# Performance work log

Measured on AMD Instinct MI355X. Metric: run time of the kernel, lower is better.

## Reference

```python
import jax, jax.numpy as jnp
import numpy as np
from jax import lax


def _mdlstm_dir(x, Wx, Wh, Wv, b):
    # x: [H, W, B, Cin]; one diagonal-causal 2D-LSTM scan (top-left origin).
    H, W, B, Cin = x.shape
    C = Wh.shape[0]
    xa = jnp.einsum('hwbi,ic->hwbc', x, Wx) + b  # [H,W,B,5C] precomputed input gates

    def col_step(carry, inp):
        h_l, c_l = carry                    # left neighbor [B,C]
        xa_ij, h_u, c_u = inp               # input preact, up neighbor
        a = xa_ij + h_l @ Wh + h_u @ Wv     # [B,5C]
        i, f1, f2, o, g = jnp.split(a, 5, axis=-1)
        c = jax.nn.sigmoid(i) * jnp.tanh(g) + jax.nn.sigmoid(f1) * c_l + jax.nn.sigmoid(f2) * c_u
        h = jax.nn.sigmoid(o) * jnp.tanh(c)
        return (h, c), (h, c)

    z = jnp.zeros((B, C), x.dtype)
    zrow = jnp.zeros((W, B, C), x.dtype)

    def row_step(carry, xa_row):
        h_up, c_up = carry                  # [W,B,C]
        _, (hs, cs) = lax.scan(col_step, (z, z), (xa_row, h_up, c_up))
        return (hs, cs), hs

    _, hh = lax.scan(row_step, (zrow, zrow), xa)  # [H,W,B,C]
    return hh


def _mdlstm4(x, Wx, Wh, Wv, b):
    # x: [B,Cin,H,W] -> per-direction outputs [4,H,W,B,C] (directions: TL, TR, BL, BR origins)
    xt = jnp.transpose(x, (2, 3, 0, 1))  # [H,W,B,Cin]
    x4 = jnp.stack([xt, xt[:, ::-1], xt[::-1], xt[::-1, ::-1]])
    o = jax.vmap(_mdlstm_dir)(x4, Wx, Wh, Wv, b)  # [4,H,W,B,C]
    return jnp.stack([o[0], o[1][:, ::-1], o[2][::-1], o[3][::-1, ::-1]])


def _block(x, Wx, Wh, Wv, b, cw, cb):
    h4 = _mdlstm4(x, Wx, Wh, Wv, b)            # [4,H,W,B,C]
    h = jnp.transpose(h4.sum(0), (2, 3, 0, 1))  # sum directions -> [B,C,H,W]
    y = lax.conv_general_dilated(h, cw, window_strides=(2, 2), padding='VALID',
                                 dimension_numbers=('NCHW', 'OIHW', 'NCHW'))
    return jnp.tanh(y + cb[None, :, None, None])


def _forward(x, p0_Wx, p0_Wh, p0_Wv, p0_b, c0_w, c0_b,
             p1_Wx, p1_Wh, p1_Wv, p1_b, c1_w, c1_b,
             p2_Wx, p2_Wh, p2_Wv, p2_b, dW, db):
    x = _block(x, p0_Wx, p0_Wh, p0_Wv, p0_b, c0_w, c0_b)  # [B,6,31,126]
    x = _block(x, p1_Wx, p1_Wh, p1_Wv, p1_b, c1_w, c1_b)  # [B,20,14,61]
    h4 = _mdlstm4(x, p2_Wx, p2_Wh, p2_Wv, p2_b)           # [4,H,W,B,50]
    # per-direction Linear(50->100) then sum over the 4 directions
    out = jnp.einsum('dhwbc,dcn->bhwn', h4, dW) + db.sum(0)
    return out  # [B,14,61,100]


def setup_inputs() -> dict:
    key = jax.random.key(0)
    ks = jax.random.split(key, 20)
    rn = lambda k, s, sc=0.1: jax.random.normal(k, s, jnp.float32) * sc
    return {
        'x': jax.random.normal(ks[0], (16, 1, 64, 256), jnp.float32),
        'p0_Wx': rn(ks[1], (4, 1, 10)), 'p0_Wh': rn(ks[2], (4, 2, 10)),
        'p0_Wv': rn(ks[3], (4, 2, 10)), 'p0_b': rn(ks[4], (4, 10)),
        'c0_w': rn(ks[5], (6, 2, 2, 4)), 'c0_b': rn(ks[6], (6,)),
        'p1_Wx': rn(ks[7], (4, 6, 50)), 'p1_Wh': rn(ks[8], (4, 10, 50)),
        'p1_Wv': rn(ks[9], (4, 10, 50)), 'p1_b': rn(ks[10], (4, 50)),
        'c1_w': rn(ks[11], (20, 10, 2, 4)), 'c1_b': rn(ks[12], (20,)),
        'p2_Wx': rn(ks[13], (4, 20, 250)), 'p2_Wh': rn(ks[14], (4, 50, 250)),
        'p2_Wv': rn(ks[15], (4, 50, 250)), 'p2_b': rn(ks[16], (4, 250)),
        'dW': rn(ks[17], (4, 50, 100)), 'db': rn(ks[18], (4, 100)),
    }


def reference(x, p0_Wx, p0_Wh, p0_Wv, p0_b, c0_w, c0_b,
              p1_Wx, p1_Wh, p1_Wv, p1_b, c1_w, c1_b,
              p2_Wx, p2_Wh, p2_Wv, p2_b, dW, db):
    return _forward(x, p0_Wx, p0_Wh, p0_Wv, p0_b, c0_w, c0_b,
                    p1_Wx, p1_Wh, p1_Wv, p1_b, c1_w, c1_b,
                    p2_Wx, p2_Wh, p2_Wv, p2_b, dW, db)
```

## Files before the change

### kernel.cpp

```cpp
#include <hip/hip_runtime.h>

typedef unsigned short ushort_t;
typedef __attribute__((ext_vector_type(8))) short short8;
typedef __attribute__((ext_vector_type(4))) float float4_t;
typedef __attribute__((ext_vector_type(2))) float v2f;

__device__ __forceinline__ float frcp(float x) { return __builtin_amdgcn_rcpf(x); }
__device__ __forceinline__ float fsig(float x) { return frcp(1.f + __expf(-x)); }
__device__ __forceinline__ float ftanh(float x) { return 1.f - 2.f * frcp(1.f + __expf(2.f * x)); }
__device__ __forceinline__ float sig_e2(float a) { return frcp(1.f + __builtin_amdgcn_exp2f(a)); }
__device__ __forceinline__ float th_e2(float a) { return 1.f - 2.f * frcp(1.f + __builtin_amdgcn_exp2f(a)); }

__device__ __forceinline__ ushort_t f2bf(float f) {
    union { float f; unsigned u; } v; v.f = f;
    unsigned u = v.u;
    unsigned r = (u + 0x7fffu + ((u >> 16) & 1u)) >> 16;
    return (ushort_t)r;
}
__device__ __forceinline__ float bf2f(ushort_t s) {
    union { unsigned u; float f; } v; v.u = ((unsigned)s) << 16;
    return v.f;
}
__device__ __forceinline__ float dpp_shr1(float x) {
    int i = __builtin_bit_cast(int, x);
    int r = __builtin_amdgcn_update_dpp(0, i, 0x138 , 0xf, 0xf, true);
    return __builtin_bit_cast(float, r);
}

__device__ __forceinline__ void barrier_lds() {
    asm volatile("s_waitcnt lgkmcnt(0)" ::: "memory");
    __builtin_amdgcn_s_barrier();
    asm volatile("" ::: "memory");
}

__global__ __launch_bounds__(128) void k_mdlstm0(
    const float* __restrict__ x, const float* __restrict__ Wx,
    const float* __restrict__ Wh, const float* __restrict__ Wv,
    const float* __restrict__ bias, float* __restrict__ h0)
{
    const int dir = blockIdx.x >> 4, b = blockIdx.x & 15;
    const int tid = threadIdx.x;
    const int u = tid >> 6;
    const int lane = tid & 63;
    const bool fH = dir >= 2, fW = (dir & 1) != 0;
    const int ri = fH ? 63 - lane : lane;
    const float L2E = 1.44269504088896340736f;

    __shared__ float Xs[64 * 256];
    __shared__ float hbuf[2][2][64];
    {
        const float* xg = x + b * 64 * 256;
        for (int i4 = tid; i4 < 4096; i4 += 128) {
            int row = i4 >> 6, c4 = (i4 & 63) << 2;
            float4 v = *(const float4*)(xg + (row << 8) + c4);
            *(float4*)&Xs[(row << 8) + c4] = v;
        }
        for (int i = tid; i < 256; i += 128) ((float*)hbuf)[i] = 0.f;
    }
    __syncthreads();

    float wx[5], bs[5], whS[5], whO[5], wvS[5], wvO[5];
#pragma unroll
    for (int g = 0; g < 5; g++) {
        float sc = (g == 4) ? 2.f * L2E : -L2E;
        int n = g * 2 + u;
        wx[g]  = Wx[dir * 10 + n] * sc;
        bs[g]  = bias[dir * 10 + n] * sc;
        whS[g] = Wh[(dir * 2 + u) * 10 + n] * sc;
        whO[g] = Wh[(dir * 2 + (1 - u)) * 10 + n] * sc;
        wvS[g] = Wv[(dir * 2 + u) * 10 + n] * sc;
        wvO[g] = Wv[(dir * 2 + (1 - u)) * 10 + n] * sc;
    }

    float* orow = h0 + (((dir * 16 + b) * 64 + ri) * 256) * 2 + u;
    float hr = 0.f, cr = 0.f;

    auto ld = [&](int d) -> float {
        int j = d - lane; j = j < 0 ? 0 : (j > 255 ? 255 : j);
        int cj = fW ? 255 - j : j;
        return Xs[(ri << 8) + cj];
    };
    float xp0 = ld(0), xp1 = ld(1);

    int p = 0;
    for (int d = 0; d < 319; d++) {
        float xv = xp0;
        xp0 = xp1;
        xp1 = ld(d + 2);

        float ho  = hbuf[p][1 - u][lane];
        float hus = dpp_shr1(hr);
        float cu  = dpp_shr1(cr);
        float huo = dpp_shr1(ho);

        int j = d - lane;
        if (j >= 0 && j < 256) {
            float a[5];
#pragma unroll
            for (int g = 0; g < 5; g++) {
                float t = fmaf(xv, wx[g], bs[g]);
                t = fmaf(hr,  whS[g], t);
                t = fmaf(ho,  whO[g], t);
                t = fmaf(hus, wvS[g], t);
                t = fmaf(huo, wvO[g], t);
                a[g] = t;
            }
            float si  = sig_e2(a[0]);
            float sf1 = sig_e2(a[1]);
            float sf2 = sig_e2(a[2]);
            float so  = sig_e2(a[3]);
            float tg  = th_e2(a[4]);
            float cn = si * tg + sf1 * cr + sf2 * cu;
            float tc = th_e2(cn * (2.f * L2E));
            hr = so * tc;
            cr = cn;
            int cj = fW ? 255 - j : j;
            orow[cj * 2] = hr;
        } else {
            hr = 0.f;
            cr = 0.f;
        }
        hbuf[1 - p][u][lane] = hr;
        barrier_lds();
        p ^= 1;
    }
}

__global__ __launch_bounds__(128) void k_conv0(
    const float* __restrict__ h0, const float* __restrict__ cw,
    const float* __restrict__ cb, float* __restrict__ x1)
{
    int blk = blockIdx.x;
    int oh = blk / 127, ow = blk % 127;
    int t = threadIdx.x;
    if (t >= 96) return;
    int b = t / 6, co = t % 6;
    float w[2][2][4];
#pragma unroll
    for (int ci = 0; ci < 2; ci++)
#pragma unroll
        for (int kh = 0; kh < 2; kh++)
#pragma unroll
            for (int kw = 0; kw < 4; kw++)
                w[ci][kh][kw] = cw[((co * 2 + ci) * 2 + kh) * 4 + kw];
    float acc = cb[co];
    for (int dirb = 0; dirb < 4; dirb++) {
#pragma unroll
        for (int kh = 0; kh < 2; kh++) {
#pragma unroll
            for (int kw = 0; kw < 4; kw++) {
                const float* ptr = h0 + ((((dirb * 16 + b) * 64) + (2 * oh + kh)) * 256 + (2 * ow + kw)) * 2;
                float2 hv = *(const float2*)ptr;
                acc = fmaf(hv.x, w[0][kh][kw], acc);
                acc = fmaf(hv.y, w[1][kh][kw], acc);
            }
        }
    }
    x1[((oh * 127 + ow) * 16 + b) * 6 + co] = ftanh(acc);
}

__global__ __launch_bounds__(768, 1) void k_mdlstm1(
    const float* __restrict__ x1, const float* __restrict__ Wx,
    const float* __restrict__ Wh, const float* __restrict__ Wv,
    const float* __restrict__ bias, float* __restrict__ h1)
{
    const int dir = blockIdx.x >> 4, b = blockIdx.x & 15;
    const bool fH = dir >= 2, fW = (dir & 1) != 0;
    const int tid = threadIdx.x;
    const int wave = tid >> 6, lane = tid & 63;

    __shared__ float Xs1[32 * 127 * 6];
    __shared__ __align__(16) ushort_t Ah[2][32][40];
    __shared__ __align__(16) ushort_t Al[2][32][40];
    __shared__ float P[32][68];
    __shared__ float cbuf[2][33][12];

    for (int i = tid; i < 2 * 32 * 40; i += 768) { ((ushort_t*)Ah)[i] = 0; ((ushort_t*)Al)[i] = 0; }
    for (int i = tid; i < 2 * 33 * 12; i += 768) ((float*)cbuf)[i] = 0.f;
    for (int i = tid; i < 32 * 127 * 6; i += 768)
        Xs1[i] = x1[(i / 6) * 96 + b * 6 + (i % 6)];
    __syncthreads();
    if (tid < 6) {
        int rr = fH ? 31 : 0, cc = fW ? 126 : 0;
        float xv = Xs1[(rr * 127 + cc) * 6 + tid];
        ushort_t xh = f2bf(xv);
        Ah[0][0][20 + tid] = xh;
        Al[0][0][20 + tid] = f2bf(xv - bf2f(xh));
    }

    const int mt = wave & 1, nt = wave >> 1;
    short8 bh = {0,0,0,0,0,0,0,0}, bl = {0,0,0,0,0,0,0,0};
    if (wave < 8) {
        int n = nt * 16 + (lane & 15);
#pragma unroll
        for (int jj = 0; jj < 8; jj++) {
            int k = (lane >> 4) * 8 + jj;
            float v = 0.f;
            if (n < 50) {
                if (k < 10)      v = Wh[(dir * 10 + k) * 50 + n];
                else if (k < 20) v = Wv[(dir * 10 + (k - 10)) * 50 + n];
                else if (k < 26) v = Wx[(dir * 6 + (k - 20)) * 50 + n];
            }
            ushort_t hi = f2bf(v);
            bh[jj] = (short)hi;
            bl[jj] = (short)f2bf(v - bf2f(hi));
        }
    }

    const int cell = tid / 10, u = tid % 10;
    float br[5];
#pragma unroll
    for (int g = 0; g < 5; g++) br[g] = (tid < 320) ? bias[dir * 50 + g * 10 + u] : 0.f;
    const int ri = fH ? 31 - cell : cell;
    float creg = 0.f;
    __syncthreads();

    int p = 0;
    for (int d = 0; d < 158; d++) {
        if (wave < 8) {
            const int arow = mt * 16 + (lane & 15);
            const int koff = (lane >> 4) * 8;
            short8 ah = *(const short8*)&Ah[p][arow][koff];
            short8 al = *(const short8*)&Al[p][arow][koff];
            float4_t acc = {0.f, 0.f, 0.f, 0.f};
            acc = __builtin_amdgcn_mfma_f32_16x16x32_bf16(ah, bh, acc, 0, 0, 0);
            acc = __builtin_amdgcn_mfma_f32_16x16x32_bf16(al, bh, acc, 0, 0, 0);
            acc = __builtin_amdgcn_mfma_f32_16x16x32_bf16(ah, bl, acc, 0, 0, 0);
            int col = nt * 16 + (lane & 15);
            int r0 = (lane >> 4) * 4;
#pragma unroll
            for (int r = 0; r < 4; r++) P[mt * 16 + r0 + r][col] = acc[r];
        } else if (tid >= 512 && tid < 704) {
            int s = tid - 512, xc = s / 6, ci = s % 6;
            int jn = d + 1 - xc;
            if (jn >= 0 && jn < 127) {
                int rr = fH ? 31 - xc : xc, cc = fW ? 126 - jn : jn;
                float xv = Xs1[(rr * 127 + cc) * 6 + ci];
                ushort_t xh = f2bf(xv);
                Ah[1 - p][xc][20 + ci] = xh;
                Al[1 - p][xc][20 + ci] = f2bf(xv - bf2f(xh));
            }
        }
        barrier_lds();

        if (tid < 320) {
            int j = d - cell;
            if (j >= 0 && j < 127) {
                float ai  = P[cell][u]      + br[0];
                float af1 = P[cell][10 + u] + br[1];
                float af2 = P[cell][20 + u] + br[2];
                float ao  = P[cell][30 + u] + br[3];
                float ag  = P[cell][40 + u] + br[4];
                float cu = cbuf[p][cell][u];
                float cn = fsig(ai) * ftanh(ag) + fsig(af1) * creg + fsig(af2) * cu;
                float hn = fsig(ao) * ftanh(cn);
                creg = cn;
                cbuf[1 - p][cell + 1][u] = cn;
                ushort_t hh = f2bf(hn);
                float hhf = bf2f(hh);
                ushort_t hlo = f2bf(hn - hhf);
                Ah[1 - p][cell][u] = hh;
                Al[1 - p][cell][u] = hlo;
                if (cell < 31) { Ah[1 - p][cell + 1][10 + u] = hh; Al[1 - p][cell + 1][10 + u] = hlo; }
                int cj = fW ? 126 - j : j;
                h1[(((dir * 16 + b) * 32 + ri) * 127 + cj) * 10 + u] = hn;
            }
        }
        barrier_lds();
        p ^= 1;
    }
}

__global__ __launch_bounds__(320, 1) void k_conv1(
    const float* __restrict__ h1, const float* __restrict__ cw,
    const float* __restrict__ cb, float* __restrict__ x2)
{
    int blk = blockIdx.x;
    int oh = blk / 62, ow = blk % 62;
    int t = threadIdx.x;
    int b = t / 20, co = t % 20;
    float w[10][2][4];
#pragma unroll
    for (int ci = 0; ci < 10; ci++)
#pragma unroll
        for (int kh = 0; kh < 2; kh++)
#pragma unroll
            for (int kw = 0; kw < 4; kw++)
                w[ci][kh][kw] = cw[((co * 10 + ci) * 2 + kh) * 4 + kw];
    float acc = cb[co];
    for (int dirb = 0; dirb < 4; dirb++) {
#pragma unroll
        for (int kh = 0; kh < 2; kh++) {
#pragma unroll
            for (int kw = 0; kw < 4; kw++) {
                const float* ptr = h1 + ((((dirb * 16 + b) * 32) + (2 * oh + kh)) * 127 + (2 * ow + kw)) * 10;
#pragma unroll
                for (int ci = 0; ci < 10; ci++)
                    acc = fmaf(ptr[ci], w[ci][kh][kw], acc);
            }
        }
    }
    x2[((oh * 62 + ow) * 16 + b) * 20 + co] = ftanh(acc);
}

__global__ __launch_bounds__(256) void k_prepB2(
    const float* __restrict__ Wh, const float* __restrict__ Wv,
    const float* __restrict__ Wx, ushort_t* __restrict__ Bh,
    ushort_t* __restrict__ Bl)
{
    int idx = blockIdx.x * 256 + threadIdx.x;
    if (idx >= 131072) return;
    int dir = idx >> 15; int k = (idx >> 8) & 127; int n = idx & 255;
    float v = 0.f;
    if (n < 250) {
        if (k < 50)       v = Wh[(dir * 50 + k) * 250 + n];
        else if (k < 100) v = Wv[(dir * 50 + (k - 50)) * 250 + n];
        else if (k < 120) v = Wx[(dir * 20 + (k - 100)) * 250 + n];
    }
    ushort_t hi = f2bf(v);
    Bh[idx] = hi;
    Bl[idx] = f2bf(v - bf2f(hi));
}

__global__ __launch_bounds__(512, 1) void k_mdlstm2(
    const float* __restrict__ x2, const ushort_t* __restrict__ BmH,
    const ushort_t* __restrict__ BmL,
    const float* __restrict__ bias, float* __restrict__ h2)
{
    const int dir = blockIdx.x >> 4, b = blockIdx.x & 15;
    const bool fH = dir >= 2, fW = (dir & 1) != 0;
    const int tid = threadIdx.x;
    const int wave = tid >> 6, lane = tid & 63;

    __shared__ float Xs2[16 * 62 * 20];
    __shared__ __align__(16) ushort_t Ah[2][16][136];
    __shared__ __align__(16) ushort_t Al[2][16][136];
    __shared__ float P[16][260];
    __shared__ float cbuf[2][16][52];

    for (int i = tid; i < 2 * 16 * 136; i += 512) { ((ushort_t*)Ah)[i] = 0; ((ushort_t*)Al)[i] = 0; }
    for (int i = tid; i < 16 * 62 * 20; i += 512)
        Xs2[i] = x2[(i / 20) * 320 + b * 20 + (i % 20)];
    __syncthreads();
    if (tid < 20) {
        int ci = tid;
        int rr = fH ? 15 : 0, cc = fW ? 61 : 0;
        float xv = Xs2[(rr * 62 + cc) * 20 + ci];
        ushort_t xh = f2bf(xv);
        Ah[0][0][100 + ci] = xh;
        Al[0][0][100 + ci] = f2bf(xv - bf2f(xh));
    }

    short8 bfragH[4][4], bfragL[4][4];
    if (wave < 4) {
#pragma unroll
        for (int j = 0; j < 4; j++) {
            const int n = wave * 64 + j * 16 + (lane & 15);
#pragma unroll
            for (int q = 0; q < 4; q++) {
#pragma unroll
                for (int jj = 0; jj < 8; jj++) {
                    int k = q * 32 + (lane >> 4) * 8 + jj;
                    bfragH[j][q][jj] = (short)BmH[(dir * 128 + k) * 256 + n];
                    bfragL[j][q][jj] = (short)BmL[(dir * 128 + k) * 256 + n];
                }
            }
        }
    }

    const int cell0 = tid / 50, u0 = tid % 50;
    const int cell1 = (512 + tid) / 50, u1 = (512 + tid) % 50;
    float bA0 = bias[dir * 250 + u0];
    float bA1 = bias[dir * 250 + 50 + u0];
    float bA2 = bias[dir * 250 + 100 + u0];
    float bA3 = bias[dir * 250 + 150 + u0];
    float bA4 = bias[dir * 250 + 200 + u0];
    float bB0 = 0, bB1 = 0, bB2 = 0, bB3 = 0, bB4 = 0;
    if (tid < 288) {
        bB0 = bias[dir * 250 + u1];
        bB1 = bias[dir * 250 + 50 + u1];
        bB2 = bias[dir * 250 + 100 + u1];
        bB3 = bias[dir * 250 + 150 + u1];
        bB4 = bias[dir * 250 + 200 + u1];
    }
    const int rrc0 = fH ? 15 - cell0 : cell0;
    const int rrc1 = fH ? 15 - cell1 : cell1;
    float creg0 = 0.f, creg1 = 0.f;
    __syncthreads();

    int p = 0;
    for (int d = 0; d < 77; d++) {
        if (wave < 4) {
            const int arow = lane & 15;
            const int koff = (lane >> 4) * 8;
            short8 ah[4], al[4];
#pragma unroll
            for (int q = 0; q < 4; q++) {
                ah[q] = *(const short8*)&Ah[p][arow][q * 32 + koff];
                al[q] = *(const short8*)&Al[p][arow][q * 32 + koff];
            }
            float4_t acc[4];
#pragma unroll
            for (int j = 0; j < 4; j++) acc[j] = (float4_t){0.f, 0.f, 0.f, 0.f};
#pragma unroll
            for (int q = 0; q < 4; q++)
#pragma unroll
                for (int j = 0; j < 4; j++)
                    acc[j] = __builtin_amdgcn_mfma_f32_16x16x32_bf16(ah[q], bfragH[j][q], acc[j], 0, 0, 0);
#pragma unroll
            for (int q = 0; q < 4; q++)
#pragma unroll
                for (int j = 0; j < 4; j++)
                    acc[j] = __builtin_amdgcn_mfma_f32_16x16x32_bf16(al[q], bfragH[j][q], acc[j], 0, 0, 0);
#pragma unroll
            for (int q = 0; q < 4; q++)
#pragma unroll
                for (int j = 0; j < 4; j++)
                    acc[j] = __builtin_amdgcn_mfma_f32_16x16x32_bf16(ah[q], bfragL[j][q], acc[j], 0, 0, 0);
            const int r0 = (lane >> 4) * 4;
#pragma unroll
            for (int j = 0; j < 4; j++) {
                int col = wave * 64 + j * 16 + (lane & 15);
#pragma unroll
                for (int r = 0; r < 4; r++) P[r0 + r][col] = acc[j][r];
            }
        } else {
            int s = tid - 256;
#pragma unroll
            for (int it = 0; it < 2; it++) {
                int item = s + it * 256;
                if (item < 320) {
                    int xc = item / 20, ci = item % 20;
                    int jn = d + 1 - xc;
                    if (jn >= 0 && jn < 62) {
                        int rr = fH ? 15 - xc : xc, cc = fW ? 61 - jn : jn;
                        float xv = Xs2[(rr * 62 + cc) * 20 + ci];
                        ushort_t xh = f2bf(xv);
                        Ah[1 - p][xc][100 + ci] = xh;
                        Al[1 - p][xc][100 + ci] = f2bf(xv - bf2f(xh));
                    }
                }
            }
        }
        barrier_lds();

        auto gate = [&](int j, int cell, int u, int rrc,
                        float g0, float g1, float g2, float g3, float g4,
                        float& creg) {
            float ai  = P[cell][u] + g0;
            float af1 = P[cell][50 + u] + g1;
            float af2 = P[cell][100 + u] + g2;
            float ao  = P[cell][150 + u] + g3;
            float ag  = P[cell][200 + u] + g4;
            float cu = (cell == 0) ? 0.f : cbuf[p][cell - 1][u];
            float cn = fsig(ai) * ftanh(ag) + fsig(af1) * creg + fsig(af2) * cu;
            float hn = fsig(ao) * ftanh(cn);
            creg = cn;
            cbuf[1 - p][cell][u] = cn;
            ushort_t hh = f2bf(hn);
            float hhf = bf2f(hh);
            ushort_t hlo = f2bf(hn - hhf);
            Ah[1 - p][cell][u] = hh;
            Al[1 - p][cell][u] = hlo;
            if (cell < 15) { Ah[1 - p][cell + 1][50 + u] = hh; Al[1 - p][cell + 1][50 + u] = hlo; }
            int cc = fW ? 61 - j : j;
            h2[(((dir * 16 + b) * 16 + rrc) * 62 + cc) * 50 + u] = hn;
        };
        {
            int j0 = d - cell0;
            if (j0 >= 0 && j0 < 62)
                gate(j0, cell0, u0, rrc0, bA0, bA1, bA2, bA3, bA4, creg0);
            if (tid < 288) {
                int j1 = d - cell1;
                if (j1 >= 0 && j1 < 62)
                    gate(j1, cell1, u1, rrc1, bB0, bB1, bB2, bB3, bB4, creg1);
            }
        }
        barrier_lds();
        p ^= 1;
    }
}

__global__ __launch_bounds__(256) void k_final(
    const float* __restrict__ h2, const float* __restrict__ dW,
    const float* __restrict__ db, float* __restrict__ out)
{
    int blk = blockIdx.x;
    int r = blk / 62, c = blk % 62;
    int t = threadIdx.x;
    __shared__ float hb[3200];
    for (int i = t; i < 3200; i += 256) {
        int dirb = i / 800, rem = i % 800, b = rem / 50, u = rem % 50;
        hb[i] = h2[(((dirb * 16 + b) * 16 + r) * 62 + c) * 50 + u];
    }
    __syncthreads();
    for (int o = t; o < 1600; o += 256) {
        int b = o / 100, n = o % 100;
        float acc = db[n] + db[100 + n] + db[200 + n] + db[300 + n];
#pragma unroll
        for (int dirb = 0; dirb < 4; dirb++) {
            const float* hp = hb + (dirb * 16 + b) * 50;
            const float* wp = dW + dirb * 5000 + n;
#pragma unroll 10
            for (int cc2 = 0; cc2 < 50; cc2++)
                acc = fmaf(hp[cc2], wp[cc2 * 100], acc);
        }
        out[((b * 16 + r) * 62 + c) * 100 + n] = acc;
    }
}

extern "C" void kernel_launch(void* const* d_in, const int* in_sizes, int n_in,
                              void* d_out, int out_size, void* d_ws, size_t ws_size,
                              hipStream_t stream)
{
    const float* x     = (const float*)d_in[0];
    const float* p0_Wx = (const float*)d_in[1];
    const float* p0_Wh = (const float*)d_in[2];
    const float* p0_Wv = (const float*)d_in[3];
    const float* p0_b  = (const float*)d_in[4];
    const float* c0_w  = (const float*)d_in[5];
    const float* c0_b  = (const float*)d_in[6];
    const float* p1_Wx = (const float*)d_in[7];
    const float* p1_Wh = (const float*)d_in[8];
    const float* p1_Wv = (const float*)d_in[9];
    const float* p1_b  = (const float*)d_in[10];
    const float* c1_w  = (const float*)d_in[11];
    const float* c1_b  = (const float*)d_in[12];
    const float* p2_Wx = (const float*)d_in[13];
    const float* p2_Wh = (const float*)d_in[14];
    const float* p2_Wv = (const float*)d_in[15];
    const float* p2_b  = (const float*)d_in[16];
    const float* dW    = (const float*)d_in[17];
    const float* db    = (const float*)d_in[18];
    float* out = (float*)d_out;
    float* ws  = (float*)d_ws;

    float* h0 = ws;
    float* x1 = h0 + 2097152;
    float* h1 = x1 + 390144;
    float* x2 = h1 + 2600960;
    float* h2 = x2 + 317440;
    ushort_t* BmH = (ushort_t*)(h2 + 3174400);
    ushort_t* BmL = BmH + 131072;

    k_prepB2<<<512, 256, 0, stream>>>(p2_Wh, p2_Wv, p2_Wx, BmH, BmL);
    k_mdlstm0<<<64, 128, 0, stream>>>(x, p0_Wx, p0_Wh, p0_Wv, p0_b, h0);
    k_conv0<<<32 * 127, 128, 0, stream>>>(h0, c0_w, c0_b, x1);
    k_mdlstm1<<<64, 768, 0, stream>>>(x1, p1_Wx, p1_Wh, p1_Wv, p1_b, h1);
    k_conv1<<<16 * 62, 320, 0, stream>>>(h1, c1_w, c1_b, x2);
    k_mdlstm2<<<64, 512, 0, stream>>>(x2, BmH, BmL, p2_b, h2);
    k_final<<<16 * 62, 256, 0, stream>>>(h2, dW, db, out);
}
```

Baseline: 478.2 us.

## Stage conv inputs in LDS per row/batch and widen mdlstm2 to one gate per thread

Both conv kernels now give each block one output row for one batch. The block stages the needed input rows from all four directions, plus the weights, into shared memory, so the strided global reads are no longer repeated per output pixel. k_mdlstm2 grows from 512 to 832 threads so each of the 800 gate cells has its own thread instead of some threads handling two. The x-staging work is also spread over 320 threads with one item each. The wider block adds register pressure and lengthens barrier waits in the serial diagonal loop. The conv kernels launch far fewer blocks, which reduces parallelism.

```diff
diff --git a/kernel.cpp b/kernel.cpp
--- a/kernel.cpp
+++ b/kernel.cpp
@@ -126,37 +126,43 @@
     }
 }
 
-__global__ __launch_bounds__(128) void k_conv0(
+__global__ __launch_bounds__(256) void k_conv0(
     const float* __restrict__ h0, const float* __restrict__ cw,
     const float* __restrict__ cb, float* __restrict__ x1)
 {
-    int blk = blockIdx.x;
-    int oh = blk / 127, ow = blk % 127;
-    int t = threadIdx.x;
-    if (t >= 96) return;
-    int b = t / 6, co = t % 6;
-    float w[2][2][4];
-#pragma unroll
-    for (int ci = 0; ci < 2; ci++)
-#pragma unroll
-        for (int kh = 0; kh < 2; kh++)
-#pragma unroll
-            for (int kw = 0; kw < 4; kw++)
-                w[ci][kh][kw] = cw[((co * 2 + ci) * 2 + kh) * 4 + kw];
-    float acc = cb[co];
-    for (int dirb = 0; dirb < 4; dirb++) {
-#pragma unroll
-        for (int kh = 0; kh < 2; kh++) {
-#pragma unroll
-            for (int kw = 0; kw < 4; kw++) {
-                const float* ptr = h0 + ((((dirb * 16 + b) * 64) + (2 * oh + kh)) * 256 + (2 * ow + kw)) * 2;
-                float2 hv = *(const float2*)ptr;
-                acc = fmaf(hv.x, w[0][kh][kw], acc);
-                acc = fmaf(hv.y, w[1][kh][kw], acc);
-            }
-        }
-    }
-    x1[((oh * 127 + ow) * 16 + b) * 6 + co] = ftanh(acc);
+    const int oh = blockIdx.x >> 4, b = blockIdx.x & 15;
+    const int tid = threadIdx.x;
+
+    __shared__ float hs[8][512];
+    __shared__ float cws[192];
+
+    for (int i4 = tid; i4 < 1024; i4 += 256) {
+        int dk = i4 >> 7;
+        int c4 = (i4 & 127) << 2;
+        const float* src = h0 + (((dk >> 1) * 16 + b) * 64 + (2 * oh + (dk & 1))) * 512 + c4;
+        *(float4*)&hs[dk][c4] = *(const float4*)src;
+    }
+    if (tid < 192) cws[tid] = cw[tid];
+    __syncthreads();
+
+    for (int o = tid; o < 762; o += 256) {
+        int ow = o / 6, co = o % 6;
+        float acc = cb[co];
+#pragma unroll
+        for (int dirb = 0; dirb < 4; dirb++) {
+#pragma unroll
+            for (int kh = 0; kh < 2; kh++) {
+                const float* hp = &hs[dirb * 2 + kh][0];
+#pragma unroll
+                for (int kw = 0; kw < 4; kw++) {
+                    float2 hv = *(const float2*)&hp[(2 * ow + kw) * 2];
+                    acc = fmaf(hv.x, cws[((co * 2 + 0) * 2 + kh) * 4 + kw], acc);
+                    acc = fmaf(hv.y, cws[((co * 2 + 1) * 2 + kh) * 4 + kw], acc);
+                }
+            }
+        }
+        x1[((oh * 127 + ow) * 16 + b) * 6 + co] = ftanh(acc);
+    }
 }
 
 __global__ __launch_bounds__(768, 1) void k_mdlstm1(
@@ -271,36 +277,44 @@
     }
 }
 
-__global__ __launch_bounds__(320, 1) void k_conv1(
+__global__ __launch_bounds__(256) void k_conv1(
     const float* __restrict__ h1, const float* __restrict__ cw,
     const float* __restrict__ cb, float* __restrict__ x2)
 {
-    int blk = blockIdx.x;
-    int oh = blk / 62, ow = blk % 62;
-    int t = threadIdx.x;
-    int b = t / 20, co = t % 20;
-    float w[10][2][4];
-#pragma unroll
-    for (int ci = 0; ci < 10; ci++)
-#pragma unroll
-        for (int kh = 0; kh < 2; kh++)
-#pragma unroll
-            for (int kw = 0; kw < 4; kw++)
-                w[ci][kh][kw] = cw[((co * 10 + ci) * 2 + kh) * 4 + kw];
-    float acc = cb[co];
-    for (int dirb = 0; dirb < 4; dirb++) {
-#pragma unroll
-        for (int kh = 0; kh < 2; kh++) {
-#pragma unroll
-            for (int kw = 0; kw < 4; kw++) {
-                const float* ptr = h1 + ((((dirb * 16 + b) * 32) + (2 * oh + kh)) * 127 + (2 * ow + kw)) * 10;
-#pragma unroll
-                for (int ci = 0; ci < 10; ci++)
-                    acc = fmaf(ptr[ci], w[ci][kh][kw], acc);
-            }
-        }
-    }
-    x2[((oh * 62 + ow) * 16 + b) * 20 + co] = ftanh(acc);
+    const int oh = blockIdx.x >> 4, b = blockIdx.x & 15;
+    const int tid = threadIdx.x;
+
+    __shared__ float hs[8][1270];
+    __shared__ float cws[1600];
+
+    for (int i2 = tid; i2 < 5080; i2 += 256) {
+        int dk = i2 / 635;
+        int c2 = (i2 % 635) * 2;
+        const float* src = h1 + (((dk >> 1) * 16 + b) * 32 + (2 * oh + (dk & 1))) * 1270 + c2;
+        *(float2*)&hs[dk][c2] = *(const float2*)src;
+    }
+    for (int i = tid; i < 1600; i += 256) cws[i] = cw[i];
+    __syncthreads();
+
+    for (int o = tid; o < 1240; o += 256) {
+        int ow = o / 20, co = o % 20;
+        float acc = cb[co];
+#pragma unroll
+        for (int dirb = 0; dirb < 4; dirb++) {
+#pragma unroll
+            for (int kh = 0; kh < 2; kh++) {
+                const float* hp = &hs[dirb * 2 + kh][0];
+#pragma unroll
+                for (int kw = 0; kw < 4; kw++) {
+                    const float* hv = &hp[(2 * ow + kw) * 10];
+#pragma unroll
+                    for (int ci = 0; ci < 10; ci++)
+                        acc = fmaf(hv[ci], cws[((co * 10 + ci) * 2 + kh) * 4 + kw], acc);
+                }
+            }
+        }
+        x2[((oh * 62 + ow) * 16 + b) * 20 + co] = ftanh(acc);
+    }
 }
 
 __global__ __launch_bounds__(256) void k_prepB2(
@@ -322,7 +336,7 @@
     Bl[idx] = f2bf(v - bf2f(hi));
 }
 
-__global__ __launch_bounds__(512, 1) void k_mdlstm2(
+__global__ __launch_bounds__(832, 1) void k_mdlstm2(
     const float* __restrict__ x2, const ushort_t* __restrict__ BmH,
     const ushort_t* __restrict__ BmL,
     const float* __restrict__ bias, float* __restrict__ h2)
@@ -338,8 +352,8 @@
     __shared__ float P[16][260];
     __shared__ float cbuf[2][16][52];
 
-    for (int i = tid; i < 2 * 16 * 136; i += 512) { ((ushort_t*)Ah)[i] = 0; ((ushort_t*)Al)[i] = 0; }
-    for (int i = tid; i < 16 * 62 * 20; i += 512)
+    for (int i = tid; i < 2 * 16 * 136; i += 832) { ((ushort_t*)Ah)[i] = 0; ((ushort_t*)Al)[i] = 0; }
+    for (int i = tid; i < 16 * 62 * 20; i += 832)
         Xs2[i] = x2[(i / 20) * 320 + b * 20 + (i % 20)];
     __syncthreads();
     if (tid < 20) {
@@ -369,23 +383,16 @@
     }
 
     const int cell0 = tid / 50, u0 = tid % 50;
-    const int cell1 = (512 + tid) / 50, u1 = (512 + tid) % 50;
-    float bA0 = bias[dir * 250 + u0];
-    float bA1 = bias[dir * 250 + 50 + u0];
-    float bA2 = bias[dir * 250 + 100 + u0];
-    float bA3 = bias[dir * 250 + 150 + u0];
-    float bA4 = bias[dir * 250 + 200 + u0];
-    float bB0 = 0, bB1 = 0, bB2 = 0, bB3 = 0, bB4 = 0;
-    if (tid < 288) {
-        bB0 = bias[dir * 250 + u1];
-        bB1 = bias[dir * 250 + 50 + u1];
-        bB2 = bias[dir * 250 + 100 + u1];
-        bB3 = bias[dir * 250 + 150 + u1];
-        bB4 = bias[dir * 250 + 200 + u1];
+    float bA0 = 0, bA1 = 0, bA2 = 0, bA3 = 0, bA4 = 0;
+    if (tid < 800) {
+        bA0 = bias[dir * 250 + u0];
+        bA1 = bias[dir * 250 + 50 + u0];
+        bA2 = bias[dir * 250 + 100 + u0];
+        bA3 = bias[dir * 250 + 150 + u0];
+        bA4 = bias[dir * 250 + 200 + u0];
     }
     const int rrc0 = fH ? 15 - cell0 : cell0;
-    const int rrc1 = fH ? 15 - cell1 : cell1;
-    float creg0 = 0.f, creg1 = 0.f;
+    float creg0 = 0.f;
     __syncthreads();
 
     int p = 0;
@@ -424,56 +431,41 @@
 #pragma unroll
                 for (int r = 0; r < 4; r++) P[r0 + r][col] = acc[j][r];
             }
-        } else {
-            int s = tid - 256;
-#pragma unroll
-            for (int it = 0; it < 2; it++) {
-                int item = s + it * 256;
-                if (item < 320) {
-                    int xc = item / 20, ci = item % 20;
-                    int jn = d + 1 - xc;
-                    if (jn >= 0 && jn < 62) {
-                        int rr = fH ? 15 - xc : xc, cc = fW ? 61 - jn : jn;
-                        float xv = Xs2[(rr * 62 + cc) * 20 + ci];
-                        ushort_t xh = f2bf(xv);
-                        Ah[1 - p][xc][100 + ci] = xh;
-                        Al[1 - p][xc][100 + ci] = f2bf(xv - bf2f(xh));
-                    }
-                }
+        } else if (tid < 576) {
+            int item = tid - 256;
+            int xc = item / 20, ci = item % 20;
+            int jn = d + 1 - xc;
+            if (jn >= 0 && jn < 62) {
+                int rr = fH ? 15 - xc : xc, cc = fW ? 61 - jn : jn;
+                float xv = Xs2[(rr * 62 + cc) * 20 + ci];
+                ushort_t xh = f2bf(xv);
+                Ah[1 - p][xc][100 + ci] = xh;
+                Al[1 - p][xc][100 + ci] = f2bf(xv - bf2f(xh));
             }
         }
         barrier_lds();
 
-        auto gate = [&](int j, int cell, int u, int rrc,
-                        float g0, float g1, float g2, float g3, float g4,
-                        float& creg) {
-            float ai  = P[cell][u] + g0;
-            float af1 = P[cell][50 + u] + g1;
-            float af2 = P[cell][100 + u] + g2;
-            float ao  = P[cell][150 + u] + g3;
-            float ag  = P[cell][200 + u] + g4;
-            float cu = (cell == 0) ? 0.f : cbuf[p][cell - 1][u];
-            float cn = fsig(ai) * ftanh(ag) + fsig(af1) * creg + fsig(af2) * cu;
-            float hn = fsig(ao) * ftanh(cn);
-            creg = cn;
-            cbuf[1 - p][cell][u] = cn;
-            ushort_t hh = f2bf(hn);
-            float hhf = bf2f(hh);
-            ushort_t hlo = f2bf(hn - hhf);
-            Ah[1 - p][cell][u] = hh;
-            Al[1 - p][cell][u] = hlo;
-            if (cell < 15) { Ah[1 - p][cell + 1][50 + u] = hh; Al[1 - p][cell + 1][50 + u] = hlo; }
-            int cc = fW ? 61 - j : j;
-            h2[(((dir * 16 + b) * 16 + rrc) * 62 + cc) * 50 + u] = hn;
-        };
-        {
-            int j0 = d - cell0;
-            if (j0 >= 0 && j0 < 62)
-                gate(j0, cell0, u0, rrc0, bA0, bA1, bA2, bA3, bA4, creg0);
-            if (tid < 288) {
-                int j1 = d - cell1;
-                if (j1 >= 0 && j1 < 62)
-                    gate(j1, cell1, u1, rrc1, bB0, bB1, bB2, bB3, bB4, creg1);
+        if (tid < 800) {
+            int j = d - cell0;
+            if (j >= 0 && j < 62) {
+                float ai  = P[cell0][u0] + bA0;
+                float af1 = P[cell0][50 + u0] + bA1;
+                float af2 = P[cell0][100 + u0] + bA2;
+                float ao  = P[cell0][150 + u0] + bA3;
+                float ag  = P[cell0][200 + u0] + bA4;
+                float cu = (cell0 == 0) ? 0.f : cbuf[p][cell0 - 1][u0];
+                float cn = fsig(ai) * ftanh(ag) + fsig(af1) * creg0 + fsig(af2) * cu;
+                float hn = fsig(ao) * ftanh(cn);
+                creg0 = cn;
+                cbuf[1 - p][cell0][u0] = cn;
+                ushort_t hh = f2bf(hn);
+                float hhf = bf2f(hh);
+                ushort_t hlo = f2bf(hn - hhf);
+                Ah[1 - p][cell0][u0] = hh;
+                Al[1 - p][cell0][u0] = hlo;
+                if (cell0 < 15) { Ah[1 - p][cell0 + 1][50 + u0] = hh; Al[1 - p][cell0 + 1][50 + u0] = hlo; }
+                int cc = fW ? 61 - j : j;
+                h2[(((dir * 16 + b) * 16 + rrc0) * 62 + cc) * 50 + u0] = hn;
             }
         }
         barrier_lds();
@@ -545,9 +537,9 @@
 
     k_prepB2<<<512, 256, 0, stream>>>(p2_Wh, p2_Wv, p2_Wx, BmH, BmL);
     k_mdlstm0<<<64, 128, 0, stream>>>(x, p0_Wx, p0_Wh, p0_Wv, p0_b, h0);
-    k_conv0<<<32 * 127, 128, 0, stream>>>(h0, c0_w, c0_b, x1);
+    k_conv0<<<32 * 16, 256, 0, stream>>>(h0, c0_w, c0_b, x1);
     k_mdlstm1<<<64, 768, 0, stream>>>(x1, p1_Wx, p1_Wh, p1_Wv, p1_b, h1);
-    k_conv1<<<16 * 62, 320, 0, stream>>>(h1, c1_w, c1_b, x2);
-    k_mdlstm2<<<64, 512, 0, stream>>>(x2, BmH, BmL, p2_b, h2);
+    k_conv1<<<16 * 16, 256, 0, stream>>>(h1, c1_w, c1_b, x2);
+    k_mdlstm2<<<64, 832, 0, stream>>>(x2, BmH, BmL, p2_b, h2);
     k_final<<<16 * 62, 256, 0, stream>>>(h2, dW, db, out);
 }
```

Result: slower. 649.4 us (+35.8%).

## Stage conv input rows and weights in LDS, one block per output row and batch

Applied to the files above, without the earlier changes.

Both strided conv kernels now use one block per (output row, batch) instead of one block per output pixel. Each block cooperatively loads the needed input rows for all four directions, plus the conv weights, into shared memory with vectorized loads. Threads then loop over (ow, co) outputs reading from LDS. This removes redundant global reads of overlapping windows and cuts the block count, at the cost of fewer blocks (512 and 256) and possible LDS bank conflicts.

```diff
diff --git a/kernel.cpp b/kernel.cpp
--- a/kernel.cpp
+++ b/kernel.cpp
@@ -126,37 +126,43 @@
     }
 }
 
-__global__ __launch_bounds__(128) void k_conv0(
+__global__ __launch_bounds__(256) void k_conv0(
     const float* __restrict__ h0, const float* __restrict__ cw,
     const float* __restrict__ cb, float* __restrict__ x1)
 {
-    int blk = blockIdx.x;
-    int oh = blk / 127, ow = blk % 127;
-    int t = threadIdx.x;
-    if (t >= 96) return;
-    int b = t / 6, co = t % 6;
-    float w[2][2][4];
-#pragma unroll
-    for (int ci = 0; ci < 2; ci++)
-#pragma unroll
-        for (int kh = 0; kh < 2; kh++)
-#pragma unroll
-            for (int kw = 0; kw < 4; kw++)
-                w[ci][kh][kw] = cw[((co * 2 + ci) * 2 + kh) * 4 + kw];
-    float acc = cb[co];
-    for (int dirb = 0; dirb < 4; dirb++) {
-#pragma unroll
-        for (int kh = 0; kh < 2; kh++) {
-#pragma unroll
-            for (int kw = 0; kw < 4; kw++) {
-                const float* ptr = h0 + ((((dirb * 16 + b) * 64) + (2 * oh + kh)) * 256 + (2 * ow + kw)) * 2;
-                float2 hv = *(const float2*)ptr;
-                acc = fmaf(hv.x, w[0][kh][kw], acc);
-                acc = fmaf(hv.y, w[1][kh][kw], acc);
-            }
-        }
-    }
-    x1[((oh * 127 + ow) * 16 + b) * 6 + co] = ftanh(acc);
+    const int oh = blockIdx.x >> 4, b = blockIdx.x & 15;
+    const int tid = threadIdx.x;
+
+    __shared__ float hs[8][512];
+    __shared__ float cws[192];
+
+    for (int i4 = tid; i4 < 1024; i4 += 256) {
+        int dk = i4 >> 7;
+        int c4 = (i4 & 127) << 2;
+        const float* src = h0 + (((dk >> 1) * 16 + b) * 64 + (2 * oh + (dk & 1))) * 512 + c4;
+        *(float4*)&hs[dk][c4] = *(const float4*)src;
+    }
+    if (tid < 192) cws[tid] = cw[tid];
+    __syncthreads();
+
+    for (int o = tid; o < 762; o += 256) {
+        int ow = o / 6, co = o % 6;
+        float acc = cb[co];
+#pragma unroll
+        for (int dirb = 0; dirb < 4; dirb++) {
+#pragma unroll
+            for (int kh = 0; kh < 2; kh++) {
+                const float* hp = &hs[dirb * 2 + kh][0];
+#pragma unroll
+                for (int kw = 0; kw < 4; kw++) {
+                    float2 hv = *(const float2*)&hp[(2 * ow + kw) * 2];
+                    acc = fmaf(hv.x, cws[((co * 2 + 0) * 2 + kh) * 4 + kw], acc);
+                    acc = fmaf(hv.y, cws[((co * 2 + 1) * 2 + kh) * 4 + kw], acc);
+                }
+            }
+        }
+        x1[((oh * 127 + ow) * 16 + b) * 6 + co] = ftanh(acc);
+    }
 }
 
 __global__ __launch_bounds__(768, 1) void k_mdlstm1(
@@ -271,36 +277,44 @@
     }
 }
 
-__global__ __launch_bounds__(320, 1) void k_conv1(
+__global__ __launch_bounds__(256) void k_conv1(
     const float* __restrict__ h1, const float* __restrict__ cw,
     const float* __restrict__ cb, float* __restrict__ x2)
 {
-    int blk = blockIdx.x;
-    int oh = blk / 62, ow = blk % 62;
-    int t = threadIdx.x;
-    int b = t / 20, co = t % 20;
-    float w[10][2][4];
-#pragma unroll
-    for (int ci = 0; ci < 10; ci++)
-#pragma unroll
-        for (int kh = 0; kh < 2; kh++)
-#pragma unroll
-            for (int kw = 0; kw < 4; kw++)
-                w[ci][kh][kw] = cw[((co * 10 + ci) * 2 + kh) * 4 + kw];
-    float acc = cb[co];
-    for (int dirb = 0; dirb < 4; dirb++) {
-#pragma unroll
-        for (int kh = 0; kh < 2; kh++) {
-#pragma unroll
-            for (int kw = 0; kw < 4; kw++) {
-                const float* ptr = h1 + ((((dirb * 16 + b) * 32) + (2 * oh + kh)) * 127 + (2 * ow + kw)) * 10;
-#pragma unroll
-                for (int ci = 0; ci < 10; ci++)
-                    acc = fmaf(ptr[ci], w[ci][kh][kw], acc);
-            }
-        }
-    }
-    x2[((oh * 62 + ow) * 16 + b) * 20 + co] = ftanh(acc);
+    const int oh = blockIdx.x >> 4, b = blockIdx.x & 15;
+    const int tid = threadIdx.x;
+
+    __shared__ float hs[8][1270];
+    __shared__ float cws[1600];
+
+    for (int i2 = tid; i2 < 5080; i2 += 256) {
+        int dk = i2 / 635;
+        int c2 = (i2 % 635) * 2;
+        const float* src = h1 + (((dk >> 1) * 16 + b) * 32 + (2 * oh + (dk & 1))) * 1270 + c2;
+        *(float2*)&hs[dk][c2] = *(const float2*)src;
+    }
+    for (int i = tid; i < 1600; i += 256) cws[i] = cw[i];
+    __syncthreads();
+
+    for (int o = tid; o < 1240; o += 256) {
+        int ow = o / 20, co = o % 20;
+        float acc = cb[co];
+#pragma unroll
+        for (int dirb = 0; dirb < 4; dirb++) {
+#pragma unroll
+            for (int kh = 0; kh < 2; kh++) {
+                const float* hp = &hs[dirb * 2 + kh][0];
+#pragma unroll
+                for (int kw = 0; kw < 4; kw++) {
+                    const float* hv = &hp[(2 * ow + kw) * 10];
+#pragma unroll
+                    for (int ci = 0; ci < 10; ci++)
+                        acc = fmaf(hv[ci], cws[((co * 10 + ci) * 2 + kh) * 4 + kw], acc);
+                }
+            }
+        }
+        x2[((oh * 62 + ow) * 16 + b) * 20 + co] = ftanh(acc);
+    }
 }
 
 __global__ __launch_bounds__(256) void k_prepB2(
@@ -545,9 +559,9 @@
 
     k_prepB2<<<512, 256, 0, stream>>>(p2_Wh, p2_Wv, p2_Wx, BmH, BmL);
     k_mdlstm0<<<64, 128, 0, stream>>>(x, p0_Wx, p0_Wh, p0_Wv, p0_b, h0);
-    k_conv0<<<32 * 127, 128, 0, stream>>>(h0, c0_w, c0_b, x1);
+    k_conv0<<<32 * 16, 256, 0, stream>>>(h0, c0_w, c0_b, x1);
     k_mdlstm1<<<64, 768, 0, stream>>>(x1, p1_Wx, p1_Wh, p1_Wv, p1_b, h1);
-    k_conv1<<<16 * 62, 320, 0, stream>>>(h1, c1_w, c1_b, x2);
+    k_conv1<<<16 * 16, 256, 0, stream>>>(h1, c1_w, c1_b, x2);
     k_mdlstm2<<<64, 512, 0, stream>>>(x2, BmH, BmL, p2_b, h2);
     k_final<<<16 * 62, 256, 0, stream>>>(h2, dW, db, out);
 }
```

Result: faster. 466.4 us (-2.5%).
